# Optimization experiments

Hardware: AMD Instinct MI355X
Metric: run time of the kernel (lower is better)

Reference implementation:

```python
import jax, jax.numpy as jnp
import numpy as np

HEADS = 16
HEAD_DIM = 64
TOKEN_DIM = 1024
INNER = HEADS * HEAD_DIM


def setup_inputs() -> dict:
    key = jax.random.key(0)
    k1, k2, k3, k4 = jax.random.split(key, 4)
    x = jax.random.normal(k1, (2, 2048, TOKEN_DIM), dtype=jnp.float32)
    # nn.Linear(token_dim, inner*3, bias=False): weight [3*inner, token_dim]
    w_qkv = jax.random.normal(k2, (3 * INNER, TOKEN_DIM), dtype=jnp.float32) * (TOKEN_DIM ** -0.5)
    # nn.Linear(inner, token_dim): weight [token_dim, inner], bias [token_dim]
    w_out = jax.random.normal(k3, (TOKEN_DIM, INNER), dtype=jnp.float32) * (INNER ** -0.5)
    b_out = jax.random.normal(k4, (TOKEN_DIM,), dtype=jnp.float32) * 0.01
    return {"x": x, "w_qkv": w_qkv, "w_out": w_out, "b_out": b_out}


def reference(x, w_qkv, w_out, b_out):
    b, n, _ = x.shape
    scale = HEAD_DIM ** -0.5
    qkv = x @ w_qkv.T                                  # [b, n, 3*inner]
    q, k, v = jnp.split(qkv, 3, axis=-1)
    def split_heads(t):
        return t.reshape(b, n, HEADS, HEAD_DIM).transpose(0, 2, 1, 3)  # [b,h,n,d]
    q, k, v = split_heads(q), split_heads(k), split_heads(v)
    dot = jnp.einsum('bhtd,bhsd->bhts', q, k) * scale  # [b,h,n,n]
    attn = jax.nn.softmax(dot, axis=-1)
    out = jnp.einsum('bhts,bhsd->bhtd', attn, v)       # [b,h,n,d]
    out = out.transpose(0, 2, 1, 3).reshape(b, n, INNER)
    return out @ w_out.T + b_out
```

## Files before the change

kernel.cpp:

```cpp
#include <hip/hip_runtime.h>
#include <hip/hip_bf16.h>

typedef short short4v __attribute__((ext_vector_type(4)));
typedef short short8 __attribute__((ext_vector_type(8)));
typedef float float4v __attribute__((ext_vector_type(4)));

#define HEADS 16
#define HDIM 64
#define TOKDIM 1024
#define SEQ 2048
#define BATCH 2
#define BH (BATCH*HEADS)
#define MROWS (BATCH*SEQ)

__device__ __forceinline__ short f2b(float f) {
    __hip_bfloat16 h = __float2bfloat16(f);
    return *reinterpret_cast<short*>(&h);
}
__device__ __forceinline__ float b2f(short s) {
    __hip_bfloat16 h;
    *reinterpret_cast<short*>(&h) = s;
    return __bfloat162float(h);
}
__device__ __forceinline__ short8 load8_f32_bf16(const float* __restrict__ p) {
    float4v a = *(const float4v*)p;
    float4v b = *(const float4v*)(p + 4);
    short8 r;
    r[0]=f2b(a[0]); r[1]=f2b(a[1]); r[2]=f2b(a[2]); r[3]=f2b(a[3]);
    r[4]=f2b(b[0]); r[5]=f2b(b[1]); r[6]=f2b(b[2]); r[7]=f2b(b[3]);
    return r;
}
__device__ __forceinline__ int packrn(float a, float b) {
    unsigned ua = __float_as_uint(a) + 0x8000u;
    unsigned ub = __float_as_uint(b) + 0x8000u;
    return (int)__builtin_amdgcn_perm(ub, ua, 0x07060302u);
}
__device__ __forceinline__ float hexp2(float x) {
    return __builtin_amdgcn_exp2f(x);
}

__device__ __forceinline__ void stage16(const void* g, void* l) {
    __builtin_amdgcn_global_load_lds((const __attribute__((address_space(1))) void*)g,
                                     (__attribute__((address_space(3))) void*)l, 16, 0, 0);
}

__global__ __launch_bounds__(256)
void cvt_bf16(const float* __restrict__ x,  short* __restrict__ xb,  int n8x,
              const float* __restrict__ wq, short* __restrict__ wqb, int n8q,
              const float* __restrict__ wo, short* __restrict__ wob, int n8o)
{
    int i = blockIdx.x*256 + threadIdx.x;
    const float* s; short* d; int off;
    if (i < n8x)                  { s = x;  d = xb;  off = i; }
    else if (i < n8x + n8q)       { s = wq; d = wqb; off = i - n8x; }
    else if (i < n8x + n8q + n8o) { s = wo; d = wob; off = i - n8x - n8q; }
    else return;
    *(short8*)&d[(size_t)off*8] = load8_f32_bf16(&s[(size_t)off*8]);
}

template<int ABF16>
__global__ __launch_bounds__(256)
void gemm_qkv(const void* __restrict__ Ap, const short* __restrict__ Wq,
              short* __restrict__ Qo, short* __restrict__ Ko, short* __restrict__ Vto)
{
    __shared__ __align__(16) short As[128*32];
    __shared__ __align__(16) short Bs[128*32];
    const int tid  = threadIdx.x;
    const int lane = tid & 63;
    const int wave = tid >> 6;
    const int wm = wave >> 1, wn = wave & 1;
    const int m0 = blockIdx.x * 128;
    const int n0 = blockIdx.y * 128;
    const int col16 = lane & 15, quad = lane >> 4;

    const int srow = lane >> 2;
    const int scol = (lane & 3) * 8;

    float4v acc[4][4];
    #pragma unroll
    for (int i=0;i<4;i++)
        #pragma unroll
        for (int j=0;j<4;j++) acc[i][j] = (float4v){0.f,0.f,0.f,0.f};

    for (int k0 = 0; k0 < TOKDIM; k0 += 32) {
        __syncthreads();
        if (ABF16) {
            const short* A = (const short*)Ap;
            #pragma unroll
            for (int j=0;j<2;++j) {
                const int rb = (wave*2 + j) * 16;
                stage16(&A[(size_t)(m0 + rb + srow)*TOKDIM + k0 + scol], &As[rb*32]);
            }
        } else {
            const float* A = (const float*)Ap;
            #pragma unroll
            for (int s=0;s<2;++s) {
                int blk = tid + s*256;
                int r = blk >> 2, kb = blk & 3;
                *(short8*)&As[r*32 + kb*8] = load8_f32_bf16(&A[(size_t)(m0+r)*TOKDIM + k0 + kb*8]);
            }
        }
        #pragma unroll
        for (int j=0;j<2;++j) {
            const int rb = (wave*2 + j) * 16;
            stage16(&Wq[(size_t)(n0 + rb + srow)*TOKDIM + k0 + scol], &Bs[rb*32]);
        }
        __syncthreads();

        short8 af[4], bfr[4];
        #pragma unroll
        for (int i=0;i<4;i++) af[i]  = *(const short8*)&As[(wm*64 + i*16 + col16)*32 + quad*8];
        #pragma unroll
        for (int j=0;j<4;j++) bfr[j] = *(const short8*)&Bs[(wn*64 + j*16 + col16)*32 + quad*8];
        #pragma unroll
        for (int i=0;i<4;i++)
            #pragma unroll
            for (int j=0;j<4;j++)
                acc[i][j] = __builtin_amdgcn_mfma_f32_16x16x32_bf16(af[i], bfr[j], acc[i][j], 0,0,0);
    }

    #pragma unroll
    for (int i=0;i<4;i++)
        #pragma unroll
        for (int j=0;j<4;j++) {
            const int n = n0 + wn*64 + j*16 + col16;
            const int part = n >> 10;
            const int h = (n & 1023) >> 6;
            const int d = n & 63;
            const int mb = m0 + wm*64 + i*16 + quad*4;
            const int b = mb >> 11;
            const int t = mb & 2047;
            if (part == 2) {
                union { short4v s; int2 i2; } w;
                #pragma unroll
                for (int r=0;r<4;r++) w.s[r] = f2b(acc[i][j][r]);
                *(int2*)&Vto[((size_t)(b*HEADS + h)*HDIM + d)*SEQ + t] = w.i2;
            } else {
                short* dst = (part == 0) ? Qo : Ko;
                #pragma unroll
                for (int r=0;r<4;r++)
                    dst[((size_t)(b*HEADS + h)*SEQ + t + r)*HDIM + d] = f2b(acc[i][j][r]);
            }
        }
}

__global__ __launch_bounds__(256)
void gemm_out(const short* __restrict__ A, const short* __restrict__ W,
              const float* __restrict__ bias, float* __restrict__ C)
{
    __shared__ __align__(16) short As[64*32];
    __shared__ __align__(16) short Bs[128*32];
    const int tid  = threadIdx.x;
    const int lane = tid & 63;
    const int wave = tid >> 6;
    const int wm = wave >> 1, wn = wave & 1;
    const int m0 = blockIdx.x * 64;
    const int n0 = blockIdx.y * 128;
    const int col16 = lane & 15, quad = lane >> 4;

    const int srow = lane >> 2;
    const int scol = (lane & 3) * 8;

    float4v acc[2][4];
    #pragma unroll
    for (int i=0;i<2;i++)
        #pragma unroll
        for (int j=0;j<4;j++) acc[i][j] = (float4v){0.f,0.f,0.f,0.f};

    for (int k0 = 0; k0 < TOKDIM; k0 += 32) {
        __syncthreads();
        {
            const int rb = wave * 16;
            stage16(&A[(size_t)(m0 + rb + srow)*TOKDIM + k0 + scol], &As[rb*32]);
        }
        #pragma unroll
        for (int j=0;j<2;++j) {
            const int rb = (wave*2 + j) * 16;
            stage16(&W[(size_t)(n0 + rb + srow)*TOKDIM + k0 + scol], &Bs[rb*32]);
        }
        __syncthreads();

        short8 af[2], bfr[4];
        #pragma unroll
        for (int i=0;i<2;i++) af[i]  = *(const short8*)&As[(wm*32 + i*16 + col16)*32 + quad*8];
        #pragma unroll
        for (int j=0;j<4;j++) bfr[j] = *(const short8*)&Bs[(wn*64 + j*16 + col16)*32 + quad*8];
        #pragma unroll
        for (int i=0;i<2;i++)
            #pragma unroll
            for (int j=0;j<4;j++)
                acc[i][j] = __builtin_amdgcn_mfma_f32_16x16x32_bf16(af[i], bfr[j], acc[i][j], 0,0,0);
    }

    #pragma unroll
    for (int i=0;i<2;i++)
        #pragma unroll
        for (int j=0;j<4;j++) {
            const int n = n0 + wn*64 + j*16 + col16;
            const float bn = bias[n];
            #pragma unroll
            for (int r=0;r<4;r++) {
                const int m = m0 + wm*32 + i*16 + quad*4 + r;
                C[(size_t)m*TOKDIM + n] = acc[i][j][r] + bn;
            }
        }
}

#define AQB 128
#define KT  64
#define VLD 72
#define NTH 16

__global__ __launch_bounds__(256, 2)
void attn_kernel(const short* __restrict__ Q, const short* __restrict__ K,
                 const short* __restrict__ Vt, short* __restrict__ AO)
{
    __shared__ __align__(16) short SL[2*2*KT*VLD];

    const int tid   = threadIdx.x;
    const int lane  = tid & 63;
    const int wave  = tid >> 6;
    const int col16 = lane & 15, quad = lane >> 4;
    const int bh  = blockIdx.y;
    const int qh  = wave & 1;
    const int kh2 = wave >> 1;
    const int qb  = blockIdx.x*AQB + qh*64;

    const short* Qb = Q  + (size_t)bh*SEQ*HDIM;
    const short* Kb = K  + (size_t)bh*SEQ*HDIM;
    const short* Vb = Vt + (size_t)bh*HDIM*SEQ;

    short* Kcs = &SL[kh2*2*KT*VLD];
    short* Vcs = Kcs + KT*VLD;

    const int local = tid & 127;
    const int sr = local >> 1;
    const int sc = (local & 1) * 32;
    const int rho = sr & 31;
    const int kslot = (sr & 32) + ((rho & 4) << 2) + ((rho & 24) >> 1) + (rho & 3);
    const int kbase = kh2 * 1024;

    const float qscale = 0.125f * 1.44269504088896f;
    short8 qf[4][2];
    #pragma unroll
    for (int qg=0; qg<4; ++qg)
        #pragma unroll
        for (int kk=0; kk<2; ++kk) {
            short8 raw = *(const short8*)&Qb[(size_t)(qb+qg*16+col16)*HDIM + kk*32 + quad*8];
            #pragma unroll
            for (int j=0;j<8;++j) raw[j] = f2b(b2f(raw[j]) * qscale);
            qf[qg][kk] = raw;
        }

    float4v o[4][4];
    #pragma unroll
    for (int qg=0;qg<4;qg++)
        #pragma unroll
        for (int dt=0;dt<4;dt++) o[qg][dt] = (float4v){0.f,0.f,0.f,0.f};
    float lsum[4] = {0.f,0.f,0.f,0.f};

    {
        #pragma unroll
        for (int i=0;i<4;++i) {
            *(short8*)&Kcs[kslot*VLD + sc + i*8] =
                *(const short8*)&Kb[(size_t)(kbase + sr)*HDIM + sc + i*8];
            *(short8*)&Vcs[sr*VLD + sc + i*8] =
                *(const short8*)&Vb[(size_t)sr*SEQ + kbase + sc + i*8];
        }
    }
    __syncthreads();

    for (int t = 0; t < NTH; ++t) {
        short8 nk[4], nv[4];
        const bool more = (t + 1 < NTH);
        if (more) {
            const int g1 = kbase + (t+1)*KT;
            #pragma unroll
            for (int i=0;i<4;++i) {
                nk[i] = *(const short8*)&Kb[(size_t)(g1 + sr)*HDIM + sc + i*8];
                nv[i] = *(const short8*)&Vb[(size_t)sr*SEQ + g1 + sc + i*8];
            }
        }

        #pragma unroll
        for (int kk = 0; kk < 2; ++kk) {
            short8 ka[2][2];
            #pragma unroll
            for (int nt=0; nt<2; ++nt)
                #pragma unroll
                for (int kh=0; kh<2; ++kh)
                    ka[nt][kh] = *(const short8*)&Kcs[(kk*32 + nt*16 + col16)*VLD + kh*32 + quad*8];
            short8 va[4];
            #pragma unroll
            for (int dt=0; dt<4; ++dt)
                va[dt] = *(const short8*)&Vcs[(dt*16 + col16)*VLD + kk*32 + quad*8];

            #pragma unroll
            for (int qg=0; qg<4; ++qg) {
                float4v st[2];
                #pragma unroll
                for (int nt=0; nt<2; ++nt) {
                    float4v z = (float4v){0.f,0.f,0.f,0.f};
                    z = __builtin_amdgcn_mfma_f32_16x16x32_bf16(ka[nt][0], qf[qg][0], z, 0,0,0);
                    z = __builtin_amdgcn_mfma_f32_16x16x32_bf16(ka[nt][1], qf[qg][1], z, 0,0,0);
                    st[nt] = z;
                }
                union { int i[4]; short8 s8; } pb;
                float p00 = hexp2(st[0][0]), p01 = hexp2(st[0][1]);
                float p02 = hexp2(st[0][2]), p03 = hexp2(st[0][3]);
                float p10 = hexp2(st[1][0]), p11 = hexp2(st[1][1]);
                float p12 = hexp2(st[1][2]), p13 = hexp2(st[1][3]);
                lsum[qg] += ((p00+p01) + (p02+p03)) + ((p10+p11) + (p12+p13));
                pb.i[0] = packrn(p00, p01); pb.i[1] = packrn(p02, p03);
                pb.i[2] = packrn(p10, p11); pb.i[3] = packrn(p12, p13);

                #pragma unroll
                for (int dt=0; dt<4; ++dt)
                    o[qg][dt] = __builtin_amdgcn_mfma_f32_16x16x32_bf16(va[dt], pb.s8, o[qg][dt], 0,0,0);
            }
        }

        __syncthreads();
        if (more) {
            #pragma unroll
            for (int i=0;i<4;++i) {
                *(short8*)&Kcs[kslot*VLD + sc + i*8] = nk[i];
                *(short8*)&Vcs[sr*VLD + sc + i*8]    = nv[i];
            }
            __syncthreads();
        }
    }

    #pragma unroll
    for (int qg=0; qg<4; ++qg) {
        lsum[qg] += __shfl_xor(lsum[qg], 16);
        lsum[qg] += __shfl_xor(lsum[qg], 32);
    }

    float* M = (float*)SL;
    float* Mw = M + (qh*64 + lane)*68;
    if (kh2 == 1) {
        #pragma unroll
        for (int qg=0; qg<4; ++qg) {
            #pragma unroll
            for (int dt=0; dt<4; ++dt)
                *(float4v*)&Mw[(qg*4+dt)*4] = o[qg][dt];
            Mw[64+qg] = lsum[qg];
        }
    }
    __syncthreads();
    if (kh2 == 0) {
        const int b = bh >> 4, h = bh & 15;
        #pragma unroll
        for (int qg=0; qg<4; ++qg) {
            lsum[qg] += Mw[64+qg];
            const float inv = 1.0f / lsum[qg];
            const int tq = qb + qg*16 + col16;
            #pragma unroll
            for (int dt=0; dt<4; ++dt) {
                float4v ov = o[qg][dt] + *(const float4v*)&Mw[(qg*4+dt)*4];
                union { short4v s; int2 i2; } w;
                #pragma unroll
                for (int r=0;r<4;++r) w.s[r] = f2b(ov[r] * inv);
                *(int2*)&AO[((size_t)(b*SEQ + tq))*TOKDIM + h*64 + dt*16 + quad*4] = w.i2;
            }
        }
    }
}

extern "C" void kernel_launch(void* const* d_in, const int* in_sizes, int n_in,
                              void* d_out, int out_size, void* d_ws, size_t ws_size,
                              hipStream_t stream)
{
    const float* x    = (const float*)d_in[0];
    const float* wqkv = (const float*)d_in[1];
    const float* wout = (const float*)d_in[2];
    const float* bout = (const float*)d_in[3];
    float* out = (float*)d_out;

    char* ws = (char*)d_ws;
    const size_t SZ   = (size_t)BH*SEQ*HDIM*sizeof(short);
    const size_t WQB  = (size_t)3*TOKDIM*TOKDIM*sizeof(short);
    const size_t WOB  = (size_t)TOKDIM*TOKDIM*sizeof(short);
    const size_t NEED_FULL = SZ + WQB + WOB + 3*SZ;
    const bool full = ws_size >= NEED_FULL;

    short *Xb, *Wqb, *Wob, *Qt, *Kt, *Vt, *AO;
    if (full) {
        Xb  = (short*)ws;
        Wqb = (short*)(ws + SZ);
        Wob = (short*)(ws + SZ + WQB);
        Qt  = (short*)(ws + SZ + WQB + WOB);
        Kt  = Qt + SZ/2;
        Vt  = Kt + SZ/2;
        AO  = Xb;
    } else {
        Xb  = nullptr;
        Wqb = (short*)ws;
        Wob = (short*)(ws + WQB);
        Qt  = (short*)(ws + WQB + WOB);
        Kt  = Qt + SZ/2;
        Vt  = Kt + SZ/2;
        AO  = Vt + SZ/2;
    }

    const int n8x = full ? (BATCH*SEQ*TOKDIM)/8 : 0;
    const int n8q = (3*TOKDIM*TOKDIM)/8;
    const int n8o = (TOKDIM*TOKDIM)/8;
    const int cvt_blocks = (n8x + n8q + n8o + 255) / 256;
    cvt_bf16<<<cvt_blocks, 256, 0, stream>>>(x, Xb, n8x, wqkv, Wqb, n8q, wout, Wob, n8o);

    if (full)
        gemm_qkv<1><<<dim3(MROWS/128, (3*TOKDIM)/128), 256, 0, stream>>>(
            (const void*)Xb, Wqb, Qt, Kt, Vt);
    else
        gemm_qkv<0><<<dim3(MROWS/128, (3*TOKDIM)/128), 256, 0, stream>>>(
            (const void*)x, Wqb, Qt, Kt, Vt);

    attn_kernel<<<dim3(SEQ/AQB, BH), 256, 0, stream>>>(Qt, Kt, Vt, AO);

    gemm_out<<<dim3(MROWS/64, TOKDIM/128), 256, 0, stream>>>(AO, Wob, bout, out);
}
```

Measured before the change: 175.4 us.

## Split attention KV range across four wave pairs with a two-stage merge

```diff
diff --git a/kernel.cpp b/kernel.cpp
--- a/kernel.cpp
+++ b/kernel.cpp
@@ -209,13 +209,13 @@
 #define AQB 128
 #define KT  64
 #define VLD 72
-#define NTH 16
-
-__global__ __launch_bounds__(256, 2)
+#define NTH 8
+
+__global__ __launch_bounds__(512, 4)
 void attn_kernel(const short* __restrict__ Q, const short* __restrict__ K,
                  const short* __restrict__ Vt, short* __restrict__ AO)
 {
-    __shared__ __align__(16) short SL[2*2*KT*VLD];
+    __shared__ __align__(16) short SL[4*2*KT*VLD];
 
     const int tid   = threadIdx.x;
     const int lane  = tid & 63;
@@ -223,14 +223,14 @@
     const int col16 = lane & 15, quad = lane >> 4;
     const int bh  = blockIdx.y;
     const int qh  = wave & 1;
-    const int kh2 = wave >> 1;
+    const int kq  = wave >> 1;
     const int qb  = blockIdx.x*AQB + qh*64;
 
     const short* Qb = Q  + (size_t)bh*SEQ*HDIM;
     const short* Kb = K  + (size_t)bh*SEQ*HDIM;
     const short* Vb = Vt + (size_t)bh*HDIM*SEQ;
 
-    short* Kcs = &SL[kh2*2*KT*VLD];
+    short* Kcs = &SL[kq*2*KT*VLD];
     short* Vcs = Kcs + KT*VLD;
 
     const int local = tid & 127;
@@ -238,7 +238,7 @@
     const int sc = (local & 1) * 32;
     const int rho = sr & 31;
     const int kslot = (sr & 32) + ((rho & 4) << 2) + ((rho & 24) >> 1) + (rho & 3);
-    const int kbase = kh2 * 1024;
+    const int kbase = kq * 512;
 
     const float qscale = 0.125f * 1.44269504088896f;
     short8 qf[4][2];
@@ -338,8 +338,8 @@
     }
 
     float* M = (float*)SL;
-    float* Mw = M + (qh*64 + lane)*68;
-    if (kh2 == 1) {
+    if (kq >= 2) {
+        float* Mw = M + (((qh<<1) + (kq-2))*64 + lane)*68;
         #pragma unroll
         for (int qg=0; qg<4; ++qg) {
             #pragma unroll
@@ -349,16 +349,39 @@
         }
     }
     __syncthreads();
-    if (kh2 == 0) {
+    if (kq < 2) {
+        float* Mr = M + (((qh<<1) + kq)*64 + lane)*68;
+        #pragma unroll
+        for (int qg=0; qg<4; ++qg) {
+            #pragma unroll
+            for (int dt=0; dt<4; ++dt)
+                o[qg][dt] += *(const float4v*)&Mr[(qg*4+dt)*4];
+            lsum[qg] += Mr[64+qg];
+        }
+    }
+    __syncthreads();
+    if (kq == 1) {
+        float* Mw = M + (qh*64 + lane)*68;
+        #pragma unroll
+        for (int qg=0; qg<4; ++qg) {
+            #pragma unroll
+            for (int dt=0; dt<4; ++dt)
+                *(float4v*)&Mw[(qg*4+dt)*4] = o[qg][dt];
+            Mw[64+qg] = lsum[qg];
+        }
+    }
+    __syncthreads();
+    if (kq == 0) {
+        float* Mr = M + (qh*64 + lane)*68;
         const int b = bh >> 4, h = bh & 15;
         #pragma unroll
         for (int qg=0; qg<4; ++qg) {
-            lsum[qg] += Mw[64+qg];
+            lsum[qg] += Mr[64+qg];
             const float inv = 1.0f / lsum[qg];
             const int tq = qb + qg*16 + col16;
             #pragma unroll
             for (int dt=0; dt<4; ++dt) {
-                float4v ov = o[qg][dt] + *(const float4v*)&Mw[(qg*4+dt)*4];
+                float4v ov = o[qg][dt] + *(const float4v*)&Mr[(qg*4+dt)*4];
                 union { short4v s; int2 i2; } w;
                 #pragma unroll
                 for (int r=0;r<4;++r) w.s[r] = f2b(ov[r] * inv);
@@ -417,7 +440,7 @@
         gemm_qkv<0><<<dim3(MROWS/128, (3*TOKDIM)/128), 256, 0, stream>>>(
             (const void*)x, Wqb, Qt, Kt, Vt);
 
-    attn_kernel<<<dim3(SEQ/AQB, BH), 256, 0, stream>>>(Qt, Kt, Vt, AO);
+    attn_kernel<<<dim3(SEQ/AQB, BH), 512, 0, stream>>>(Qt, Kt, Vt, AO);
 
     gemm_out<<<dim3(MROWS/64, TOKDIM/128), 256, 0, stream>>>(AO, Wob, bout, out);
 }
```

Measured after the change: 465.5 us. +165.3%, slower.

## Double-buffer attention K/V tiles in LDS with direct swizzled global-to-LDS staging

Applied to the files above, without the earlier changes.

```diff
diff --git a/kernel.cpp b/kernel.cpp
--- a/kernel.cpp
+++ b/kernel.cpp
@@ -208,14 +208,15 @@
 
 #define AQB 128
 #define KT  64
-#define VLD 72
 #define NTH 16
+#define KVT (KT*HDIM)
+#define BUF2 (2*KVT)
 
 __global__ __launch_bounds__(256, 2)
 void attn_kernel(const short* __restrict__ Q, const short* __restrict__ K,
                  const short* __restrict__ Vt, short* __restrict__ AO)
 {
-    __shared__ __align__(16) short SL[2*2*KT*VLD];
+    __shared__ __align__(16) short SL[2*2*BUF2];
 
     const int tid   = threadIdx.x;
     const int lane  = tid & 63;
@@ -230,15 +231,25 @@
     const short* Kb = K  + (size_t)bh*SEQ*HDIM;
     const short* Vb = Vt + (size_t)bh*HDIM*SEQ;
 
-    short* Kcs = &SL[kh2*2*KT*VLD];
-    short* Vcs = Kcs + KT*VLD;
-
-    const int local = tid & 127;
-    const int sr = local >> 1;
-    const int sc = (local & 1) * 32;
-    const int rho = sr & 31;
-    const int kslot = (sr & 32) + ((rho & 4) << 2) + ((rho & 24) >> 1) + (rho & 3);
+    short* Sbase = &SL[kh2*2*BUF2];
     const int kbase = kh2 * 1024;
+
+    const int w   = wave & 1;
+    const int l3  = lane >> 3;
+    const int scsw = (((lane & 7) ^ l3) << 4) >> 1;
+    int krow[4], vrow[4];
+    #pragma unroll
+    for (int c=0;c<4;++c) {
+        const int s = w*32 + c*8 + l3;
+        krow[c] = (s&32) + ((s&12)<<1) + ((s&16)>>2) + (s&3);
+        vrow[c] = s;
+    }
+
+    const int r7 = col16 & 7;
+    int scol2[2];
+    #pragma unroll
+    for (int j=0;j<2;++j)
+        scol2[j] = ((((j<<6) | (quad<<4)) ^ (r7<<4)) >> 1);
 
     const float qscale = 0.125f * 1.44269504088896f;
     short8 qf[4][2];
@@ -260,25 +271,28 @@
     float lsum[4] = {0.f,0.f,0.f,0.f};
 
     {
-        #pragma unroll
-        for (int i=0;i<4;++i) {
-            *(short8*)&Kcs[kslot*VLD + sc + i*8] =
-                *(const short8*)&Kb[(size_t)(kbase + sr)*HDIM + sc + i*8];
-            *(short8*)&Vcs[sr*VLD + sc + i*8] =
-                *(const short8*)&Vb[(size_t)sr*SEQ + kbase + sc + i*8];
+        short* Kn = Sbase;
+        short* Vn = Sbase + KVT;
+        #pragma unroll
+        for (int c=0;c<4;++c) {
+            stage16(&Kb[(size_t)(kbase + krow[c])*HDIM + scsw], &Kn[w*2048 + c*512]);
+            stage16(&Vb[(size_t)vrow[c]*SEQ + kbase + scsw],    &Vn[w*2048 + c*512]);
         }
     }
     __syncthreads();
 
     for (int t = 0; t < NTH; ++t) {
-        short8 nk[4], nv[4];
-        const bool more = (t + 1 < NTH);
-        if (more) {
+        short* Kc = Sbase + (t & 1)*BUF2;
+        short* Vc = Kc + KVT;
+
+        if (t + 1 < NTH) {
             const int g1 = kbase + (t+1)*KT;
-            #pragma unroll
-            for (int i=0;i<4;++i) {
-                nk[i] = *(const short8*)&Kb[(size_t)(g1 + sr)*HDIM + sc + i*8];
-                nv[i] = *(const short8*)&Vb[(size_t)sr*SEQ + g1 + sc + i*8];
+            short* Kn = Sbase + ((t & 1)^1)*BUF2;
+            short* Vn = Kn + KVT;
+            #pragma unroll
+            for (int c=0;c<4;++c) {
+                stage16(&Kb[(size_t)(g1 + krow[c])*HDIM + scsw], &Kn[w*2048 + c*512]);
+                stage16(&Vb[(size_t)vrow[c]*SEQ + g1 + scsw],    &Vn[w*2048 + c*512]);
             }
         }
 
@@ -289,11 +303,11 @@
             for (int nt=0; nt<2; ++nt)
                 #pragma unroll
                 for (int kh=0; kh<2; ++kh)
-                    ka[nt][kh] = *(const short8*)&Kcs[(kk*32 + nt*16 + col16)*VLD + kh*32 + quad*8];
+                    ka[nt][kh] = *(const short8*)&Kc[(kk*32 + nt*16 + col16)*64 + scol2[kh]];
             short8 va[4];
             #pragma unroll
             for (int dt=0; dt<4; ++dt)
-                va[dt] = *(const short8*)&Vcs[(dt*16 + col16)*VLD + kk*32 + quad*8];
+                va[dt] = *(const short8*)&Vc[(dt*16 + col16)*64 + scol2[kk]];
 
             #pragma unroll
             for (int qg=0; qg<4; ++qg) {
@@ -321,14 +335,6 @@
         }
 
         __syncthreads();
-        if (more) {
-            #pragma unroll
-            for (int i=0;i<4;++i) {
-                *(short8*)&Kcs[kslot*VLD + sc + i*8] = nk[i];
-                *(short8*)&Vcs[sr*VLD + sc + i*8]    = nv[i];
-            }
-            __syncthreads();
-        }
     }
 
     #pragma unroll
@@ -359,10 +365,10 @@
             #pragma unroll
             for (int dt=0; dt<4; ++dt) {
                 float4v ov = o[qg][dt] + *(const float4v*)&Mw[(qg*4+dt)*4];
-                union { short4v s; int2 i2; } w;
-                #pragma unroll
-                for (int r=0;r<4;++r) w.s[r] = f2b(ov[r] * inv);
-                *(int2*)&AO[((size_t)(b*SEQ + tq))*TOKDIM + h*64 + dt*16 + quad*4] = w.i2;
+                union { short4v s; int2 i2; } w2;
+                #pragma unroll
+                for (int r=0;r<4;++r) w2.s[r] = f2b(ov[r] * inv);
+                *(int2*)&AO[((size_t)(b*SEQ + tq))*TOKDIM + h*64 + dt*16 + quad*4] = w2.i2;
             }
         }
     }
```

Result: no change. 175.2 us (-0.1%).
